# Optimization experiments

Measured on AMD Instinct MI355X. Metric: run time of the kernel, lower is better.

## Reference

```python
import jax, jax.numpy as jnp
import numpy as np

N_NODES = 100000
N_EDGES = 1600000
C_IN, C_HID, C_OUT = 32, 32, 8
N_AGENTS = 1000


def _glorot(key, shape):
    fan_in, fan_out = shape[0], shape[1]
    lim = float(np.sqrt(6.0 / (fan_in + fan_out)))
    return jax.random.uniform(key, shape, jnp.float32, -lim, lim)


def setup_inputs() -> dict:
    key = jax.random.key(0)
    ks = jax.random.split(key, 16)
    x = jax.random.normal(ks[0], (N_NODES, C_IN), jnp.float32)
    edge_index = jax.random.randint(ks[1], (2, N_EDGES), 0, N_NODES, jnp.int64)
    d = {"x": x, "edge_index": edge_index}
    dims = [(C_IN, C_HID), (C_HID, C_HID), (C_HID, C_HID)]
    for i, (di, do) in enumerate(dims, start=1):
        d[f"W_l{i}"] = _glorot(ks[2 * i], (di, do))        # neighbor (aggregated) weight
        d[f"b_l{i}"] = jnp.zeros((do,), jnp.float32)
        d[f"W_r{i}"] = _glorot(ks[2 * i + 1], (di, do))    # root/self weight (no bias)
    d["W_out"] = _glorot(ks[10], (C_HID, C_OUT))
    d["b_out"] = jnp.zeros((C_OUT,), jnp.float32)
    return d


def _sage_conv(x, src, dst, W_l, b_l, W_r):
    # mean-aggregate neighbor features at destination nodes
    msg = x[src]                                               # [E, d] gather
    summed = jax.ops.segment_sum(msg, dst, num_segments=N_NODES)
    cnt = jax.ops.segment_sum(jnp.ones((src.shape[0],), x.dtype), dst,
                              num_segments=N_NODES)
    agg = summed / jnp.maximum(cnt, 1.0)[:, None]              # deg==0 -> 0
    return agg @ W_l + b_l + x @ W_r


def reference(x, edge_index, W_l1, b_l1, W_r1, W_l2, b_l2, W_r2,
              W_l3, b_l3, W_r3, W_out, b_out):
    src, dst = edge_index[0], edge_index[1]
    h = jax.nn.relu(_sage_conv(x, src, dst, W_l1, b_l1, W_r1))
    h = jax.nn.relu(_sage_conv(h, src, dst, W_l2, b_l2, W_r2))
    h = jax.nn.relu(_sage_conv(h, src, dst, W_l3, b_l3, W_r3))
    out = h @ W_out + b_out
    return out[:N_AGENTS]
```

## Files before the change

### kernel.cpp

```cpp
#include <hip/hip_runtime.h>
#include <hip/hip_bf16.h>

#define N_NODES 100000
#define N_EDGES 1600000
#define N_AGENTS 1000

#define NB 782
#define ABLK 512
#define CHUNK (N_EDGES / ABLK)
#define CONV_BLOCKS 3125
#define FLAGS_I4 25024
#define FLAG_BLOCKS 98

typedef short s16x8 __attribute__((ext_vector_type(8)));
typedef float f32x4 __attribute__((ext_vector_type(4)));

__device__ __forceinline__ unsigned short f2bf(float f) {
    unsigned u = __float_as_uint(f);
    u += 0x7fffu + ((u >> 16) & 1u);
    return (unsigned short)(u >> 16);
}
__device__ __forceinline__ float bflo(unsigned u) { return __uint_as_float(u << 16); }
__device__ __forceinline__ float bfhi(unsigned u) { return __uint_as_float(u & 0xffff0000u); }

__global__ __launch_bounds__(256) void hist_prep_kernel(
    const int* __restrict__ dst, int* __restrict__ partialT,
    const float* __restrict__ x, unsigned short* __restrict__ xb,
    const float* __restrict__ Wl1, const float* __restrict__ Wr1,
    const float* __restrict__ Wl2, const float* __restrict__ Wr2,
    const float* __restrict__ Wl3, const float* __restrict__ Wr3,
    unsigned short* __restrict__ Wcat, int* __restrict__ flags)
{
    int b = blockIdx.x;
    if (b < ABLK) {
        __shared__ int hist[NB];
        for (int i = threadIdx.x; i < NB; i += 256) hist[i] = 0;
        __syncthreads();
        int beg = b * CHUNK;
        for (int e = beg + threadIdx.x; e < beg + CHUNK; e += 256)
            atomicAdd(&hist[dst[e] >> 7], 1);
        __syncthreads();
        for (int i = threadIdx.x; i < NB; i += 256) partialT[i * ABLK + b] = hist[i];
    } else if (b < ABLK + CONV_BLOCKS) {
        int i = (b - ABLK) * 256 + threadIdx.x;
        float4 v = ((const float4*)x)[i];
        ((ushort4*)xb)[i] = make_ushort4(f2bf(v.x), f2bf(v.y), f2bf(v.z), f2bf(v.w));
    } else if (b < ABLK + CONV_BLOCKS + 24) {
        int gid = (b - ABLK - CONV_BLOCKS) * 256 + threadIdx.x;
        int L = gid >> 11, idx = gid & 2047;
        int k = idx >> 5, n = idx & 31;
        const float* Wl = (L == 0) ? Wl1 : (L == 1) ? Wl2 : Wl3;
        const float* Wr = (L == 0) ? Wr1 : (L == 1) ? Wr2 : Wr3;
        float v = (k < 32) ? Wl[k * 32 + n] : Wr[(k - 32) * 32 + n];
        Wcat[gid] = f2bf(v);
    } else {
        int gid = (b - ABLK - CONV_BLOCKS - 24) * 256 + threadIdx.x;
        if (gid < FLAGS_I4) ((int4*)flags)[gid] = make_int4(0, 0, 0, 0);
    }
}

__global__ __launch_bounds__(256) void bucket_prefix_kernel(
    const int* __restrict__ partialT, int* __restrict__ baseT, int* __restrict__ tot)
{
    int wave = threadIdx.x >> 6, lane = threadIdx.x & 63;
    int t = blockIdx.x * 4 + wave;
    if (t >= NB) return;
    const int4* p = (const int4*)(partialT + (size_t)t * ABLK);
    int4 u0 = p[lane * 2], u1 = p[lane * 2 + 1];
    int v0 = u0.x, v1 = u0.y, v2 = u0.z, v3 = u0.w;
    int v4 = u1.x, v5 = u1.y, v6 = u1.z, v7 = u1.w;
    int p0 = 0, p1 = v0, p2 = p1 + v1, p3 = p2 + v2;
    int p4 = p3 + v3, p5 = p4 + v4, p6 = p5 + v5, p7 = p6 + v6;
    int s = p7 + v7;
    int x = s;
    #pragma unroll
    for (int off = 1; off < 64; off <<= 1) {
        int y = __shfl_up(x, off);
        if (lane >= off) x += y;
    }
    int excl = x - s;
    int4* q = (int4*)(baseT + (size_t)t * ABLK);
    q[lane * 2]     = make_int4(excl + p0, excl + p1, excl + p2, excl + p3);
    q[lane * 2 + 1] = make_int4(excl + p4, excl + p5, excl + p6, excl + p7);
    if (lane == 63) tot[t] = x;
}

__global__ __launch_bounds__(256) void bucket_scatter_kernel(
    const int* __restrict__ src, const int* __restrict__ dst,
    const int* __restrict__ baseT, const int* __restrict__ tot,
    int* __restrict__ bstart, int* __restrict__ ebuf)
{
    __shared__ int cur[NB];
    __shared__ int tsum[256];
    int b = blockIdx.x, t = threadIdx.x;
    int i0 = t * 4;
    int v0 = (i0     < NB) ? tot[i0]     : 0;
    int v1 = (i0 + 1 < NB) ? tot[i0 + 1] : 0;
    int v2 = (i0 + 2 < NB) ? tot[i0 + 2] : 0;
    int v3 = (i0 + 3 < NB) ? tot[i0 + 3] : 0;
    int p1 = v0, p2 = v0 + v1, p3 = v0 + v1 + v2, s4 = p3 + v3;
    tsum[t] = s4;
    __syncthreads();
    for (int off = 1; off < 256; off <<= 1) {
        int u = (t >= off) ? tsum[t - off] : 0;
        __syncthreads();
        tsum[t] += u;
        __syncthreads();
    }
    int excl = tsum[t] - s4;
    int st0 = excl, st1 = excl + p1, st2 = excl + p2, st3 = excl + p3;
    if (i0     < NB) cur[i0]     = st0 + baseT[(size_t)i0 * ABLK + b];
    if (i0 + 1 < NB) cur[i0 + 1] = st1 + baseT[(size_t)(i0 + 1) * ABLK + b];
    if (i0 + 2 < NB) cur[i0 + 2] = st2 + baseT[(size_t)(i0 + 2) * ABLK + b];
    if (i0 + 3 < NB) cur[i0 + 3] = st3 + baseT[(size_t)(i0 + 3) * ABLK + b];
    if (b == 0) {
        if (i0     < NB) bstart[i0]     = st0;
        if (i0 + 1 < NB) bstart[i0 + 1] = st1;
        if (i0 + 2 < NB) bstart[i0 + 2] = st2;
        if (i0 + 3 < NB) bstart[i0 + 3] = st3;
        if (t == 255)    bstart[NB] = tsum[255];
    }
    __syncthreads();
    int beg = b * CHUNK;
    for (int e = beg + threadIdx.x; e < beg + CHUNK; e += 256) {
        int d = dst[e];
        int slot = atomicAdd(&cur[d >> 7], 1);
        ebuf[slot] = src[e] | ((d & 127) << 17);
    }
}

__global__ __launch_bounds__(256) void bucket_csr_kernel(
    const int* __restrict__ bstart, const int* __restrict__ ebuf,
    unsigned* __restrict__ pk, int* __restrict__ esrc,
    int* __restrict__ flags)
{
    __shared__ int hist4[512], cur4[512], tmp[256];
    int b = blockIdx.x;
    int t = threadIdx.x;
    int beg = bstart[b], end = bstart[b + 1];
    hist4[t] = 0; hist4[t + 256] = 0;
    __syncthreads();
    for (int i = beg + t; i < end; i += 256) {
        int p = ebuf[i];
        int ln = (p >> 17) & 127;
        int cls = (p & 0x1FFFF) >> 15;
        atomicAdd(&hist4[ln * 4 + cls], 1);
    }
    __syncthreads();
    int c0 = 0, c1 = 0, c2 = 0, c3 = 0, v = 0;
    if (t < 128) {
        c0 = hist4[t * 4 + 0]; c1 = hist4[t * 4 + 1];
        c2 = hist4[t * 4 + 2]; c3 = hist4[t * 4 + 3];
        v = c0 + c1 + c2 + c3;
    }
    tmp[t] = v;
    __syncthreads();
    for (int off = 1; off < 256; off <<= 1) {
        int u = (t >= off) ? tmp[t - off] : 0;
        __syncthreads();
        tmp[t] += u;
        __syncthreads();
    }
    int excl = tmp[t] - v;
    int node = b * 128 + t;
    if (t < 128 && node < N_NODES) {
        int start = beg + excl;
        pk[node] = ((unsigned)start << 11) | (unsigned)min(v, 2047);
        cur4[t * 4 + 0] = start;
        cur4[t * 4 + 1] = start + c0;
        cur4[t * 4 + 2] = start + c0 + c1;
        cur4[t * 4 + 3] = start + c0 + c1 + c2;
        if (node < N_AGENTS) flags[node] = 1;
    }
    __syncthreads();
    bool agent_bucket = (b < 8);
    for (int i = beg + t; i < end; i += 256) {
        int p = ebuf[i];
        int ln = (p >> 17) & 127;
        int s = p & 0x1FFFF;
        int slot = atomicAdd(&cur4[ln * 4 + (s >> 15)], 1);
        esrc[slot] = s;
        if (agent_bucket && (b * 128 + ln) < N_AGENTS)
            flags[s] = 1;
    }
}

__global__ __launch_bounds__(256) void sage_fused_kernel(
    const unsigned* __restrict__ pk, const int* __restrict__ esrc,
    const unsigned short* __restrict__ hb,
    const unsigned short* __restrict__ Wcat, const float* __restrict__ bl,
    const float* __restrict__ Wout, const float* __restrict__ bout,
    void* __restrict__ outp, int n_nodes, int final)
{
    __shared__ unsigned short sW[2048];
    __shared__ float sb[32];
    __shared__ unsigned short smean[64 * 40];
    __shared__ float sh3[64 * 33];
    __shared__ float sWo[256];
    __shared__ float sbo[8];

    int tid = threadIdx.x;
    ((uint4*)sW)[tid] = ((const uint4*)Wcat)[tid];
    if (tid < 32) sb[tid] = bl[tid];
    if (final) {
        sWo[tid] = Wout[tid];
        if (tid < 8) sbo[tid] = bout[tid];
    }

    int lane = tid & 63, wave = tid >> 6;

    int g = lane >> 2, q = lane & 3;
    int nodeA = blockIdx.x * 64 + wave * 16 + g;
    int beg = 0, cnt = 0;
    if (nodeA < n_nodes) {
        unsigned pkv = pk[nodeA];
        beg = (int)(pkv >> 11);
        cnt = (int)(pkv & 2047u);
    }
    int end = beg + cnt;
    float a0 = 0.f, a1 = 0.f, a2 = 0.f, a3 = 0.f;
    float a4 = 0.f, a5 = 0.f, a6 = 0.f, a7 = 0.f;
    int j = beg;
    for (; j + 3 < end; j += 4) {
        int s0 = esrc[j];
        int s1 = esrc[j + 1];
        int s2 = esrc[j + 2];
        int s3 = esrc[j + 3];
        uint4 u0 = *(const uint4*)(hb + s0 * 32 + q * 8);
        uint4 u1 = *(const uint4*)(hb + s1 * 32 + q * 8);
        uint4 u2 = *(const uint4*)(hb + s2 * 32 + q * 8);
        uint4 u3 = *(const uint4*)(hb + s3 * 32 + q * 8);
        a0 += bflo(u0.x); a1 += bfhi(u0.x);
        a2 += bflo(u0.y); a3 += bfhi(u0.y);
        a4 += bflo(u0.z); a5 += bfhi(u0.z);
        a6 += bflo(u0.w); a7 += bfhi(u0.w);
        a0 += bflo(u1.x); a1 += bfhi(u1.x);
        a2 += bflo(u1.y); a3 += bfhi(u1.y);
        a4 += bflo(u1.z); a5 += bfhi(u1.z);
        a6 += bflo(u1.w); a7 += bfhi(u1.w);
        a0 += bflo(u2.x); a1 += bfhi(u2.x);
        a2 += bflo(u2.y); a3 += bfhi(u2.y);
        a4 += bflo(u2.z); a5 += bfhi(u2.z);
        a6 += bflo(u2.w); a7 += bfhi(u2.w);
        a0 += bflo(u3.x); a1 += bfhi(u3.x);
        a2 += bflo(u3.y); a3 += bfhi(u3.y);
        a4 += bflo(u3.z); a5 += bfhi(u3.z);
        a6 += bflo(u3.w); a7 += bfhi(u3.w);
    }
    for (; j < end; j++) {
        int s = esrc[j];
        uint4 u = *(const uint4*)(hb + s * 32 + q * 8);
        a0 += bflo(u.x); a1 += bfhi(u.x);
        a2 += bflo(u.y); a3 += bfhi(u.y);
        a4 += bflo(u.z); a5 += bfhi(u.z);
        a6 += bflo(u.w); a7 += bfhi(u.w);
    }
    float iv = 1.0f / fmaxf((float)cnt, 1.0f);
    uint4 o;
    o.x = (unsigned)f2bf(a0 * iv) | ((unsigned)f2bf(a1 * iv) << 16);
    o.y = (unsigned)f2bf(a2 * iv) | ((unsigned)f2bf(a3 * iv) << 16);
    o.z = (unsigned)f2bf(a4 * iv) | ((unsigned)f2bf(a5 * iv) << 16);
    o.w = (unsigned)f2bf(a6 * iv) | ((unsigned)f2bf(a7 * iv) << 16);
    int mrow = wave * 16 + g;
    *(uint4*)&smean[mrow * 40 + q * 8] = o;
    __syncthreads();

    int l15 = lane & 15, quad = lane >> 4;
    s16x8 bf_[2][2];
    #pragma unroll
    for (int kt = 0; kt < 2; kt++)
        #pragma unroll
        for (int nt = 0; nt < 2; nt++)
            #pragma unroll
            for (int jj = 0; jj < 8; jj++) {
                int k = kt * 32 + quad * 8 + jj;
                bf_[kt][nt][jj] = (short)sW[k * 32 + l15 + nt * 16];
            }
    float bias0 = sb[l15], bias1 = sb[l15 + 16];

    int tilebase = blockIdx.x * 64 + wave * 16;
    int nodeD = tilebase + l15;
    int na = min(nodeD, n_nodes - 1);
    s16x8 am = *(const s16x8*)&smean[(wave * 16 + l15) * 40 + quad * 8];
    s16x8 as = *(const s16x8*)(hb + (size_t)na * 32 + quad * 8);
    f32x4 acc0 = {0.f, 0.f, 0.f, 0.f};
    f32x4 acc1 = {0.f, 0.f, 0.f, 0.f};
    acc0 = __builtin_amdgcn_mfma_f32_16x16x32_bf16(am, bf_[0][0], acc0, 0, 0, 0);
    acc0 = __builtin_amdgcn_mfma_f32_16x16x32_bf16(as, bf_[1][0], acc0, 0, 0, 0);
    acc1 = __builtin_amdgcn_mfma_f32_16x16x32_bf16(am, bf_[0][1], acc1, 0, 0, 0);
    acc1 = __builtin_amdgcn_mfma_f32_16x16x32_bf16(as, bf_[1][1], acc1, 0, 0, 0);

    if (!final) {
        #pragma unroll
        for (int r = 0; r < 4; r++) {
            int onode = tilebase + quad * 4 + r;
            if (onode < n_nodes) {
                ((unsigned short*)outp)[onode * 32 + l15]      = f2bf(fmaxf(acc0[r] + bias0, 0.f));
                ((unsigned short*)outp)[onode * 32 + l15 + 16] = f2bf(fmaxf(acc1[r] + bias1, 0.f));
            }
        }
    } else {
        #pragma unroll
        for (int r = 0; r < 4; r++) {
            int row = wave * 16 + quad * 4 + r;
            sh3[row * 33 + l15]      = fmaxf(acc0[r] + bias0, 0.f);
            sh3[row * 33 + l15 + 16] = fmaxf(acc1[r] + bias1, 0.f);
        }
        __syncthreads();
        #pragma unroll
        for (int i = tid; i < 512; i += 256) {
            int ln = i >> 3, c = i & 7;
            int gn = blockIdx.x * 64 + ln;
            if (gn < N_AGENTS) {
                float ov = sbo[c];
                #pragma unroll
                for (int k = 0; k < 32; k++) ov += sh3[ln * 33 + k] * sWo[k * 8 + c];
                ((float*)outp)[gn * 8 + c] = ov;
            }
        }
    }
}

__global__ __launch_bounds__(256) void sage_fused_flag_kernel(
    const unsigned* __restrict__ pk, const int* __restrict__ esrc,
    const unsigned short* __restrict__ hb,
    const unsigned short* __restrict__ Wcat, const float* __restrict__ bl,
    unsigned short* __restrict__ outp, const int* __restrict__ flags,
    int n_nodes)
{
    __shared__ unsigned short sW[2048];
    __shared__ float sb[32];
    __shared__ unsigned short smean[64 * 40];
    __shared__ int sflag[64];

    int tid = threadIdx.x;
    ((uint4*)sW)[tid] = ((const uint4*)Wcat)[tid];
    if (tid < 32) sb[tid] = bl[tid];
    if (tid < 64) {
        int gid = blockIdx.x * 64 + tid;
        sflag[tid] = (gid < n_nodes) ? flags[gid] : 0;
    }
    __syncthreads();

    int lane = tid & 63, wave = tid >> 6;

    int g = lane >> 2, q = lane & 3;
    int lnode = wave * 16 + g;
    int nodeA = blockIdx.x * 64 + lnode;
    int beg = 0, cnt = 0;
    if (sflag[lnode]) {
        unsigned pkv = pk[nodeA];
        beg = (int)(pkv >> 11);
        cnt = (int)(pkv & 2047u);
    }
    int end = beg + cnt;
    float a0 = 0.f, a1 = 0.f, a2 = 0.f, a3 = 0.f;
    float a4 = 0.f, a5 = 0.f, a6 = 0.f, a7 = 0.f;
    int j = beg;
    for (; j + 3 < end; j += 4) {
        int s0 = esrc[j];
        int s1 = esrc[j + 1];
        int s2 = esrc[j + 2];
        int s3 = esrc[j + 3];
        uint4 u0 = *(const uint4*)(hb + s0 * 32 + q * 8);
        uint4 u1 = *(const uint4*)(hb + s1 * 32 + q * 8);
        uint4 u2 = *(const uint4*)(hb + s2 * 32 + q * 8);
        uint4 u3 = *(const uint4*)(hb + s3 * 32 + q * 8);
        a0 += bflo(u0.x); a1 += bfhi(u0.x);
        a2 += bflo(u0.y); a3 += bfhi(u0.y);
        a4 += bflo(u0.z); a5 += bfhi(u0.z);
        a6 += bflo(u0.w); a7 += bfhi(u0.w);
        a0 += bflo(u1.x); a1 += bfhi(u1.x);
        a2 += bflo(u1.y); a3 += bfhi(u1.y);
        a4 += bflo(u1.z); a5 += bfhi(u1.z);
        a6 += bflo(u1.w); a7 += bfhi(u1.w);
        a0 += bflo(u2.x); a1 += bfhi(u2.x);
        a2 += bflo(u2.y); a3 += bfhi(u2.y);
        a4 += bflo(u2.z); a5 += bfhi(u2.z);
        a6 += bflo(u2.w); a7 += bfhi(u2.w);
        a0 += bflo(u3.x); a1 += bfhi(u3.x);
        a2 += bflo(u3.y); a3 += bfhi(u3.y);
        a4 += bflo(u3.z); a5 += bfhi(u3.z);
        a6 += bflo(u3.w); a7 += bfhi(u3.w);
    }
    for (; j < end; j++) {
        int s = esrc[j];
        uint4 u = *(const uint4*)(hb + s * 32 + q * 8);
        a0 += bflo(u.x); a1 += bfhi(u.x);
        a2 += bflo(u.y); a3 += bfhi(u.y);
        a4 += bflo(u.z); a5 += bfhi(u.z);
        a6 += bflo(u.w); a7 += bfhi(u.w);
    }
    float iv = 1.0f / fmaxf((float)cnt, 1.0f);
    uint4 o;
    o.x = (unsigned)f2bf(a0 * iv) | ((unsigned)f2bf(a1 * iv) << 16);
    o.y = (unsigned)f2bf(a2 * iv) | ((unsigned)f2bf(a3 * iv) << 16);
    o.z = (unsigned)f2bf(a4 * iv) | ((unsigned)f2bf(a5 * iv) << 16);
    o.w = (unsigned)f2bf(a6 * iv) | ((unsigned)f2bf(a7 * iv) << 16);
    *(uint4*)&smean[lnode * 40 + q * 8] = o;
    __syncthreads();

    int l15 = lane & 15, quad = lane >> 4;
    s16x8 bf_[2][2];
    #pragma unroll
    for (int kt = 0; kt < 2; kt++)
        #pragma unroll
        for (int nt = 0; nt < 2; nt++)
            #pragma unroll
            for (int jj = 0; jj < 8; jj++) {
                int k = kt * 32 + quad * 8 + jj;
                bf_[kt][nt][jj] = (short)sW[k * 32 + l15 + nt * 16];
            }
    float bias0 = sb[l15], bias1 = sb[l15 + 16];

    int tilebase = blockIdx.x * 64 + wave * 16;
    int nodeD = tilebase + l15;
    int na = min(nodeD, n_nodes - 1);
    s16x8 am = *(const s16x8*)&smean[(wave * 16 + l15) * 40 + quad * 8];
    s16x8 as = *(const s16x8*)(hb + (size_t)na * 32 + quad * 8);
    f32x4 acc0 = {0.f, 0.f, 0.f, 0.f};
    f32x4 acc1 = {0.f, 0.f, 0.f, 0.f};
    acc0 = __builtin_amdgcn_mfma_f32_16x16x32_bf16(am, bf_[0][0], acc0, 0, 0, 0);
    acc0 = __builtin_amdgcn_mfma_f32_16x16x32_bf16(as, bf_[1][0], acc0, 0, 0, 0);
    acc1 = __builtin_amdgcn_mfma_f32_16x16x32_bf16(am, bf_[0][1], acc1, 0, 0, 0);
    acc1 = __builtin_amdgcn_mfma_f32_16x16x32_bf16(as, bf_[1][1], acc1, 0, 0, 0);

    #pragma unroll
    for (int r = 0; r < 4; r++) {
        int lr = wave * 16 + quad * 4 + r;
        int onode = tilebase + quad * 4 + r;
        if (onode < n_nodes && sflag[lr]) {
            outp[onode * 32 + l15]      = f2bf(fmaxf(acc0[r] + bias0, 0.f));
            outp[onode * 32 + l15 + 16] = f2bf(fmaxf(acc1[r] + bias1, 0.f));
        }
    }
}

extern "C" void kernel_launch(void* const* d_in, const int* in_sizes, int n_in,
                              void* d_out, int out_size, void* d_ws, size_t ws_size,
                              hipStream_t stream) {
    const float* x   = (const float*)d_in[0];
    const int* ei    = (const int*)d_in[1];
    const float* Wl1 = (const float*)d_in[2];
    const float* bl1 = (const float*)d_in[3];
    const float* Wr1 = (const float*)d_in[4];
    const float* Wl2 = (const float*)d_in[5];
    const float* bl2 = (const float*)d_in[6];
    const float* Wr2 = (const float*)d_in[7];
    const float* Wl3 = (const float*)d_in[8];
    const float* bl3 = (const float*)d_in[9];
    const float* Wr3 = (const float*)d_in[10];
    const float* Wout = (const float*)d_in[11];
    const float* bout = (const float*)d_in[12];
    float* out = (float*)d_out;

    const int* src = ei;
    const int* dst = ei + N_EDGES;

    char* ws = (char*)d_ws;
    unsigned* pk    = (unsigned*)ws;                           ws += (size_t)100096 * 4;
    int*   partialT = (int*)ws;                                ws += (size_t)NB * ABLK * 4;
    int*   baseT    = (int*)ws;                                ws += (size_t)NB * ABLK * 4;
    int*   tot      = (int*)ws;                                ws += 784 * 4;
    int*   bstart   = (int*)ws;                                ws += 784 * 4;
    int*   esrc     = (int*)ws;                                ws += (size_t)N_EDGES * 4;
    unsigned short* hXb   = (unsigned short*)ws;               ws += (size_t)N_NODES * 32 * 2;
    unsigned short* hAb   = (unsigned short*)ws;               ws += (size_t)N_NODES * 32 * 2;
    unsigned short* hBb   = (unsigned short*)ws;               ws += (size_t)N_NODES * 32 * 2;
    unsigned short* Wcat  = (unsigned short*)ws;               ws += 3 * 2048 * 2;
    int*   flags    = (int*)ws;                                ws += (size_t)100096 * 4;
    int*   ebuf     = (int*)hAb;

    hist_prep_kernel<<<ABLK + CONV_BLOCKS + 24 + FLAG_BLOCKS, 256, 0, stream>>>(
        dst, partialT, x, hXb, Wl1, Wr1, Wl2, Wr2, Wl3, Wr3, Wcat, flags);
    bucket_prefix_kernel<<<(NB + 3) / 4, 256, 0, stream>>>(partialT, baseT, tot);
    bucket_scatter_kernel<<<ABLK, 256, 0, stream>>>(src, dst, baseT, tot, bstart, ebuf);
    bucket_csr_kernel<<<NB, 256, 0, stream>>>(bstart, ebuf, pk, esrc, flags);

    sage_fused_kernel<<<(N_NODES + 63) / 64, 256, 0, stream>>>(
        pk, esrc, hXb, Wcat, bl1, Wout, bout, hAb, N_NODES, 0);
    sage_fused_flag_kernel<<<(N_NODES + 63) / 64, 256, 0, stream>>>(
        pk, esrc, hAb, Wcat + 2048, bl2, hBb, flags, N_NODES);
    sage_fused_kernel<<<(N_AGENTS + 63) / 64, 256, 0, stream>>>(
        pk, esrc, hBb, Wcat + 4096, bl3, Wout, bout, out, N_AGENTS, 1);
}
```

Before: 177.5 us.

## Coalesce histogram writes, swizzle scatter chunk order, unroll gather loop by eight

The histogram kernel now writes per-block partial counts row-major (block-major with padded stride), so each block's stores are contiguous; the prefix kernel reads them strided instead. The scatter kernel remaps block index to chunk with a swizzle, likely to spread concurrently running blocks across the edge range or XCDs. The neighbor gather loops in the fused SAGE kernels are unrolled to eight outstanding loads per iteration to raise memory-level parallelism, at the cost of more registers.

```diff
diff --git a/kernel.cpp b/kernel.cpp
--- a/kernel.cpp
+++ b/kernel.cpp
@@ -6,6 +6,7 @@
 #define N_AGENTS 1000
 
 #define NB 782
+#define NBP 800
 #define ABLK 512
 #define CHUNK (N_EDGES / ABLK)
 #define CONV_BLOCKS 3125
@@ -22,6 +23,12 @@
 }
 __device__ __forceinline__ float bflo(unsigned u) { return __uint_as_float(u << 16); }
 __device__ __forceinline__ float bfhi(unsigned u) { return __uint_as_float(u & 0xffff0000u); }
+
+#define ACC8(U) do { \
+    a0 += bflo(U.x); a1 += bfhi(U.x); \
+    a2 += bflo(U.y); a3 += bfhi(U.y); \
+    a4 += bflo(U.z); a5 += bfhi(U.z); \
+    a6 += bflo(U.w); a7 += bfhi(U.w); } while (0)
 
 __global__ __launch_bounds__(256) void hist_prep_kernel(
     const int* __restrict__ dst, int* __restrict__ partialT,
@@ -40,7 +47,7 @@
         for (int e = beg + threadIdx.x; e < beg + CHUNK; e += 256)
             atomicAdd(&hist[dst[e] >> 7], 1);
         __syncthreads();
-        for (int i = threadIdx.x; i < NB; i += 256) partialT[i * ABLK + b] = hist[i];
+        for (int i = threadIdx.x; i < NB; i += 256) partialT[b * NBP + i] = hist[i];
     } else if (b < ABLK + CONV_BLOCKS) {
         int i = (b - ABLK) * 256 + threadIdx.x;
         float4 v = ((const float4*)x)[i];
@@ -65,10 +72,15 @@
     int wave = threadIdx.x >> 6, lane = threadIdx.x & 63;
     int t = blockIdx.x * 4 + wave;
     if (t >= NB) return;
-    const int4* p = (const int4*)(partialT + (size_t)t * ABLK);
-    int4 u0 = p[lane * 2], u1 = p[lane * 2 + 1];
-    int v0 = u0.x, v1 = u0.y, v2 = u0.z, v3 = u0.w;
-    int v4 = u1.x, v5 = u1.y, v6 = u1.z, v7 = u1.w;
+    int c0i = lane * 8;
+    int v0 = partialT[(c0i + 0) * NBP + t];
+    int v1 = partialT[(c0i + 1) * NBP + t];
+    int v2 = partialT[(c0i + 2) * NBP + t];
+    int v3 = partialT[(c0i + 3) * NBP + t];
+    int v4 = partialT[(c0i + 4) * NBP + t];
+    int v5 = partialT[(c0i + 5) * NBP + t];
+    int v6 = partialT[(c0i + 6) * NBP + t];
+    int v7 = partialT[(c0i + 7) * NBP + t];
     int p0 = 0, p1 = v0, p2 = p1 + v1, p3 = p2 + v2;
     int p4 = p3 + v3, p5 = p4 + v4, p6 = p5 + v5, p7 = p6 + v6;
     int s = p7 + v7;
@@ -93,6 +105,7 @@
     __shared__ int cur[NB];
     __shared__ int tsum[256];
     int b = blockIdx.x, t = threadIdx.x;
+    int chunk = ((b & 7) << 6) | (b >> 3);
     int i0 = t * 4;
     int v0 = (i0     < NB) ? tot[i0]     : 0;
     int v1 = (i0 + 1 < NB) ? tot[i0 + 1] : 0;
@@ -109,10 +122,10 @@
     }
     int excl = tsum[t] - s4;
     int st0 = excl, st1 = excl + p1, st2 = excl + p2, st3 = excl + p3;
-    if (i0     < NB) cur[i0]     = st0 + baseT[(size_t)i0 * ABLK + b];
-    if (i0 + 1 < NB) cur[i0 + 1] = st1 + baseT[(size_t)(i0 + 1) * ABLK + b];
-    if (i0 + 2 < NB) cur[i0 + 2] = st2 + baseT[(size_t)(i0 + 2) * ABLK + b];
-    if (i0 + 3 < NB) cur[i0 + 3] = st3 + baseT[(size_t)(i0 + 3) * ABLK + b];
+    if (i0     < NB) cur[i0]     = st0 + baseT[(size_t)i0 * ABLK + chunk];
+    if (i0 + 1 < NB) cur[i0 + 1] = st1 + baseT[(size_t)(i0 + 1) * ABLK + chunk];
+    if (i0 + 2 < NB) cur[i0 + 2] = st2 + baseT[(size_t)(i0 + 2) * ABLK + chunk];
+    if (i0 + 3 < NB) cur[i0 + 3] = st3 + baseT[(size_t)(i0 + 3) * ABLK + chunk];
     if (b == 0) {
         if (i0     < NB) bstart[i0]     = st0;
         if (i0 + 1 < NB) bstart[i0 + 1] = st1;
@@ -121,7 +134,7 @@
         if (t == 255)    bstart[NB] = tsum[255];
     }
     __syncthreads();
-    int beg = b * CHUNK;
+    int beg = chunk * CHUNK;
     for (int e = beg + threadIdx.x; e < beg + CHUNK; e += 256) {
         int d = dst[e];
         int slot = atomicAdd(&cur[d >> 7], 1);
@@ -221,39 +234,32 @@
     float a0 = 0.f, a1 = 0.f, a2 = 0.f, a3 = 0.f;
     float a4 = 0.f, a5 = 0.f, a6 = 0.f, a7 = 0.f;
     int j = beg;
-    for (; j + 3 < end; j += 4) {
-        int s0 = esrc[j];
-        int s1 = esrc[j + 1];
-        int s2 = esrc[j + 2];
-        int s3 = esrc[j + 3];
+    for (; j + 7 < end; j += 8) {
+        int s0 = esrc[j],     s1 = esrc[j + 1], s2 = esrc[j + 2], s3 = esrc[j + 3];
+        int s4 = esrc[j + 4], s5 = esrc[j + 5], s6 = esrc[j + 6], s7 = esrc[j + 7];
         uint4 u0 = *(const uint4*)(hb + s0 * 32 + q * 8);
         uint4 u1 = *(const uint4*)(hb + s1 * 32 + q * 8);
         uint4 u2 = *(const uint4*)(hb + s2 * 32 + q * 8);
         uint4 u3 = *(const uint4*)(hb + s3 * 32 + q * 8);
-        a0 += bflo(u0.x); a1 += bfhi(u0.x);
-        a2 += bflo(u0.y); a3 += bfhi(u0.y);
-        a4 += bflo(u0.z); a5 += bfhi(u0.z);
-        a6 += bflo(u0.w); a7 += bfhi(u0.w);
-        a0 += bflo(u1.x); a1 += bfhi(u1.x);
-        a2 += bflo(u1.y); a3 += bfhi(u1.y);
-        a4 += bflo(u1.z); a5 += bfhi(u1.z);
-        a6 += bflo(u1.w); a7 += bfhi(u1.w);
-        a0 += bflo(u2.x); a1 += bfhi(u2.x);
-        a2 += bflo(u2.y); a3 += bfhi(u2.y);
-        a4 += bflo(u2.z); a5 += bfhi(u2.z);
-        a6 += bflo(u2.w); a7 += bfhi(u2.w);
-        a0 += bflo(u3.x); a1 += bfhi(u3.x);
-        a2 += bflo(u3.y); a3 += bfhi(u3.y);
-        a4 += bflo(u3.z); a5 += bfhi(u3.z);
-        a6 += bflo(u3.w); a7 += bfhi(u3.w);
+        uint4 u4 = *(const uint4*)(hb + s4 * 32 + q * 8);
+        uint4 u5 = *(const uint4*)(hb + s5 * 32 + q * 8);
+        uint4 u6 = *(const uint4*)(hb + s6 * 32 + q * 8);
+        uint4 u7 = *(const uint4*)(hb + s7 * 32 + q * 8);
+        ACC8(u0); ACC8(u1); ACC8(u2); ACC8(u3);
+        ACC8(u4); ACC8(u5); ACC8(u6); ACC8(u7);
+    }
+    for (; j + 3 < end; j += 4) {
+        int s0 = esrc[j], s1 = esrc[j + 1], s2 = esrc[j + 2], s3 = esrc[j + 3];
+        uint4 u0 = *(const uint4*)(hb + s0 * 32 + q * 8);
+        uint4 u1 = *(const uint4*)(hb + s1 * 32 + q * 8);
+        uint4 u2 = *(const uint4*)(hb + s2 * 32 + q * 8);
+        uint4 u3 = *(const uint4*)(hb + s3 * 32 + q * 8);
+        ACC8(u0); ACC8(u1); ACC8(u2); ACC8(u3);
     }
     for (; j < end; j++) {
         int s = esrc[j];
         uint4 u = *(const uint4*)(hb + s * 32 + q * 8);
-        a0 += bflo(u.x); a1 += bfhi(u.x);
-        a2 += bflo(u.y); a3 += bfhi(u.y);
-        a4 += bflo(u.z); a5 += bfhi(u.z);
-        a6 += bflo(u.w); a7 += bfhi(u.w);
+        ACC8(u);
     }
     float iv = 1.0f / fmaxf((float)cnt, 1.0f);
     uint4 o;
@@ -357,39 +363,32 @@
     float a0 = 0.f, a1 = 0.f, a2 = 0.f, a3 = 0.f;
     float a4 = 0.f, a5 = 0.f, a6 = 0.f, a7 = 0.f;
     int j = beg;
-    for (; j + 3 < end; j += 4) {
-        int s0 = esrc[j];
-        int s1 = esrc[j + 1];
-        int s2 = esrc[j + 2];
-        int s3 = esrc[j + 3];
+    for (; j + 7 < end; j += 8) {
+        int s0 = esrc[j],     s1 = esrc[j + 1], s2 = esrc[j + 2], s3 = esrc[j + 3];
+        int s4 = esrc[j + 4], s5 = esrc[j + 5], s6 = esrc[j + 6], s7 = esrc[j + 7];
         uint4 u0 = *(const uint4*)(hb + s0 * 32 + q * 8);
         uint4 u1 = *(const uint4*)(hb + s1 * 32 + q * 8);
         uint4 u2 = *(const uint4*)(hb + s2 * 32 + q * 8);
         uint4 u3 = *(const uint4*)(hb + s3 * 32 + q * 8);
-        a0 += bflo(u0.x); a1 += bfhi(u0.x);
-        a2 += bflo(u0.y); a3 += bfhi(u0.y);
-        a4 += bflo(u0.z); a5 += bfhi(u0.z);
-        a6 += bflo(u0.w); a7 += bfhi(u0.w);
-        a0 += bflo(u1.x); a1 += bfhi(u1.x);
-        a2 += bflo(u1.y); a3 += bfhi(u1.y);
-        a4 += bflo(u1.z); a5 += bfhi(u1.z);
-        a6 += bflo(u1.w); a7 += bfhi(u1.w);
-        a0 += bflo(u2.x); a1 += bfhi(u2.x);
-        a2 += bflo(u2.y); a3 += bfhi(u2.y);
-        a4 += bflo(u2.z); a5 += bfhi(u2.z);
-        a6 += bflo(u2.w); a7 += bfhi(u2.w);
-        a0 += bflo(u3.x); a1 += bfhi(u3.x);
-        a2 += bflo(u3.y); a3 += bfhi(u3.y);
-        a4 += bflo(u3.z); a5 += bfhi(u3.z);
-        a6 += bflo(u3.w); a7 += bfhi(u3.w);
+        uint4 u4 = *(const uint4*)(hb + s4 * 32 + q * 8);
+        uint4 u5 = *(const uint4*)(hb + s5 * 32 + q * 8);
+        uint4 u6 = *(const uint4*)(hb + s6 * 32 + q * 8);
+        uint4 u7 = *(const uint4*)(hb + s7 * 32 + q * 8);
+        ACC8(u0); ACC8(u1); ACC8(u2); ACC8(u3);
+        ACC8(u4); ACC8(u5); ACC8(u6); ACC8(u7);
+    }
+    for (; j + 3 < end; j += 4) {
+        int s0 = esrc[j], s1 = esrc[j + 1], s2 = esrc[j + 2], s3 = esrc[j + 3];
+        uint4 u0 = *(const uint4*)(hb + s0 * 32 + q * 8);
+        uint4 u1 = *(const uint4*)(hb + s1 * 32 + q * 8);
+        uint4 u2 = *(const uint4*)(hb + s2 * 32 + q * 8);
+        uint4 u3 = *(const uint4*)(hb + s3 * 32 + q * 8);
+        ACC8(u0); ACC8(u1); ACC8(u2); ACC8(u3);
     }
     for (; j < end; j++) {
         int s = esrc[j];
         uint4 u = *(const uint4*)(hb + s * 32 + q * 8);
-        a0 += bflo(u.x); a1 += bfhi(u.x);
-        a2 += bflo(u.y); a3 += bfhi(u.y);
-        a4 += bflo(u.z); a5 += bfhi(u.z);
-        a6 += bflo(u.w); a7 += bfhi(u.w);
+        ACC8(u);
     }
     float iv = 1.0f / fmaxf((float)cnt, 1.0f);
     uint4 o;
@@ -459,7 +458,7 @@
 
     char* ws = (char*)d_ws;
     unsigned* pk    = (unsigned*)ws;                           ws += (size_t)100096 * 4;
-    int*   partialT = (int*)ws;                                ws += (size_t)NB * ABLK * 4;
+    int*   partialT = (int*)ws;                                ws += (size_t)ABLK * NBP * 4;
     int*   baseT    = (int*)ws;                                ws += (size_t)NB * ABLK * 4;
     int*   tot      = (int*)ws;                                ws += 784 * 4;
     int*   bstart   = (int*)ws;                                ws += 784 * 4;
```

Result: no change. 175.4 us (median of 2 runs) (-1.2%).
